# Kernel optimization log

Measured on AMD Instinct MI355X. Metric: run time of the kernel, lower is better.

Reference implementation:

```python
import jax, jax.numpy as jnp
import numpy as np

N = 100000   # nodes
E = 3200000  # edges (before self-loops)
G = 256      # graphs in batch
IN_DIM, HID, OUT3 = 25, 64, 32


def setup_inputs() -> dict:
    key = jax.random.key(0)
    ks = jax.random.split(key, 13)
    def w(k, shape, fan_in):
        return jax.random.normal(k, shape, jnp.float32) * (1.0 / np.sqrt(fan_in))
    return {
        "x": jax.random.normal(ks[0], (N, IN_DIM), jnp.float32),
        "edge_index": jax.random.randint(ks[1], (2, E), 0, N, dtype=jnp.int32),
        "batch": jnp.sort(jax.random.randint(ks[2], (N,), 0, G, dtype=jnp.int32)),
        "W1": w(ks[3], (IN_DIM, HID), IN_DIM), "b1": jnp.zeros((HID,), jnp.float32),
        "W2": w(ks[4], (HID, HID), HID),       "b2": jnp.zeros((HID,), jnp.float32),
        "W3": w(ks[5], (HID, OUT3), HID),      "b3": jnp.zeros((OUT3,), jnp.float32),
        "Wh1": w(ks[6], (OUT3, 32), OUT3),     "bh1": jnp.zeros((32,), jnp.float32),
        "Wh2": w(ks[7], (32, 1), 32),          "bh2": jnp.zeros((1,), jnp.float32),
    }


def _gcn_layer(x, W, b, src, dst, num_nodes):
    # GCNConv: h = W^T x; out_i = sum_j norm_ij * h_j (+ self-loop), norm = d_i^-1/2 d_j^-1/2
    h = x @ W  # [N, F_out]
    ones = jnp.ones(src.shape[0], h.dtype)
    deg = jax.ops.segment_sum(ones, dst, num_segments=num_nodes)  # includes self-loops -> >= 1
    dinv = jax.lax.rsqrt(jnp.maximum(deg, 1.0))
    norm = dinv[src] * dinv[dst]                       # [E+N]
    msgs = h[src] * norm[:, None]                       # gather + scale
    out = jax.ops.segment_sum(msgs, dst, num_segments=num_nodes)  # scatter-add
    return out + b


def reference(x, edge_index, batch, W1, b1, W2, b2, W3, b3, Wh1, bh1, Wh2, bh2):
    n = x.shape[0]
    loops = jnp.arange(n, dtype=edge_index.dtype)
    src = jnp.concatenate([edge_index[0], loops])  # add self-loops
    dst = jnp.concatenate([edge_index[1], loops])

    h = jax.nn.relu(_gcn_layer(x, W1, b1, src, dst, n))
    h = jax.nn.relu(_gcn_layer(h, W2, b2, src, dst, n))
    h = jax.nn.relu(_gcn_layer(h, W3, b3, src, dst, n))

    # global mean pool over graphs
    counts = jax.ops.segment_sum(jnp.ones(n, h.dtype), batch, num_segments=G)
    g = jax.ops.segment_sum(h, batch, num_segments=G) / jnp.maximum(counts, 1.0)[:, None]

    y = jax.nn.relu(g @ Wh1 + bh1) @ Wh2 + bh2  # [G, 1]
    return y.squeeze(-1)
```

## Files before the change

kernel.cpp:

```cpp
#include <hip/hip_runtime.h>
#include <hip/hip_fp16.h>


#define IN_DIM 25
#define HID 64
#define OUT3 32
#define BK_LOG 6
#define BK_NODES 64
#define MAXB 2048
#define NPT 8
#define EPB1 16384
#define BCAP 4096
#define RNG_LOG 14
#define NR 8
#define NKEY (BK_NODES * NR)

__global__ __launch_bounds__(256) void bucket_hist(const int* __restrict__ dst,
                                                   int* __restrict__ bhist, int nE) {
    __shared__ int h[MAXB];
    for (int i = threadIdx.x; i < MAXB; i += 256) h[i] = 0;
    __syncthreads();
    int e0 = blockIdx.x * 8192;
    int cnt = min(8192, nE - e0);
    for (int i = threadIdx.x; i < cnt; i += 256)
        atomicAdd(&h[(unsigned)dst[e0 + i] >> BK_LOG], 1);
    __syncthreads();
    for (int i = threadIdx.x; i < MAXB; i += 256)
        if (h[i]) atomicAdd(&bhist[i], h[i]);
}

__global__ __launch_bounds__(256) void bucket_scan(const int* __restrict__ bhist,
                                                   int* __restrict__ bbase,
                                                   int* __restrict__ cursor,
                                                   int nb, int nE) {
    __shared__ int s4[256];
    int t = threadIdx.x;
    int v[NPT]; int sum = 0;
#pragma unroll
    for (int j = 0; j < NPT; ++j) {
        int b = NPT * t + j;
        v[j] = (b < nb) ? bhist[b] : 0;
        sum += v[j];
    }
    s4[t] = sum;
    __syncthreads();
    for (int off = 1; off < 256; off <<= 1) {
        int mine = s4[t];
        int add = (t >= off) ? s4[t - off] : 0;
        __syncthreads();
        s4[t] = mine + add;
        __syncthreads();
    }
    int run = s4[t] - sum;
#pragma unroll
    for (int j = 0; j < NPT; ++j) {
        int b = NPT * t + j;
        if (b < nb) { bbase[b] = run; cursor[b] = run; }
        run += v[j];
    }
    if (t == 0) bbase[nb] = nE;
}

__global__ __launch_bounds__(256) void partition_kernel(
        const int* __restrict__ src, const int* __restrict__ dst,
        int* __restrict__ cursor, unsigned int* __restrict__ ebuf, int nE) {
    __shared__ int lh[MAXB];
    __shared__ int lrun[MAXB];
    __shared__ int lcur[MAXB];
    __shared__ int swp[256];
    __shared__ unsigned int stg[EPB1];
    __shared__ unsigned short sbk[EPB1];
    int t = threadIdx.x;
    int e0 = blockIdx.x * EPB1;
    int cnt = min(EPB1, nE - e0);
    for (int i = t; i < MAXB; i += 256) lh[i] = 0;
    __syncthreads();
    for (int i = t; i < cnt; i += 256)
        atomicAdd(&lh[(unsigned)dst[e0 + i] >> BK_LOG], 1);
    __syncthreads();
    int v[NPT]; int sum = 0;
#pragma unroll
    for (int j = 0; j < NPT; ++j) { v[j] = lh[NPT * t + j]; sum += v[j]; }
    swp[t] = sum;
    __syncthreads();
    for (int off = 1; off < 256; off <<= 1) {
        int mine = swp[t];
        int add = (t >= off) ? swp[t - off] : 0;
        __syncthreads();
        swp[t] = mine + add;
        __syncthreads();
    }
    int run = swp[t] - sum;
#pragma unroll
    for (int j = 0; j < NPT; ++j) {
        int b = NPT * t + j;
        lh[b] = run;
        lcur[b] = 0;
        if (v[j] > 0) lrun[b] = atomicAdd(&cursor[b], v[j]);
        run += v[j];
    }
    __syncthreads();
    for (int i = t; i < cnt; i += 256) {
        int d = dst[e0 + i];
        int s = src[e0 + i];
        int b = (unsigned)d >> BK_LOG;
        int lp = atomicAdd(&lcur[b], 1);
        int slot = lh[b] + lp;
        stg[slot] = ((unsigned)(d & (BK_NODES - 1)) << 17) | (unsigned)s;
        sbk[slot] = (unsigned short)b;
    }
    __syncthreads();
    for (int i = t; i < cnt; i += 256) {
        int b = sbk[i];
        int g = lrun[b] + (i - lh[b]);
        ebuf[g] = stg[i];
    }
}

__global__ __launch_bounds__(256) void bucket_csr_kernel(
        unsigned int* __restrict__ ebuf, const int* __restrict__ bbase,
        float* __restrict__ dinv, int* __restrict__ gp64, int* __restrict__ gp32,
        int nN) {
    int b = blockIdx.x;
    int node_lo = b << BK_LOG;
    int nn = min(BK_NODES, nN - node_lo);
    int base = bbase[b];
    int cnt = bbase[b + 1] - base;
    if (cnt > BCAP) cnt = BCAP;
    __shared__ unsigned int in[BCAP];
    __shared__ unsigned int outb[BCAP];
    __shared__ int h[NKEY], sc[NKEY], lc[NKEY];
    __shared__ int swp[256];
    int t = threadIdx.x;
    for (int i = t; i < cnt; i += 256) in[i] = ebuf[base + i];
    for (int i = t; i < NKEY; i += 256) { h[i] = 0; lc[i] = 0; }
    __syncthreads();
    for (int i = t; i < cnt; i += 256) {
        unsigned int w = in[i];
        int kk = (int)(((w & 0x1FFFFu) >> RNG_LOG) << BK_LOG) | (int)(w >> 17);
        atomicAdd(&h[kk], 1);
    }
    __syncthreads();
    int v[2]; int sum = 0;
#pragma unroll
    for (int j = 0; j < 2; ++j) { v[j] = h[2 * t + j]; sum += v[j]; }
    swp[t] = sum;
    __syncthreads();
    for (int off = 1; off < 256; off <<= 1) {
        int mine = swp[t];
        int add = (t >= off) ? swp[t - off] : 0;
        __syncthreads();
        swp[t] = mine + add;
        __syncthreads();
    }
    int run = swp[t] - sum;
#pragma unroll
    for (int j = 0; j < 2; ++j) { sc[2 * t + j] = run; run += v[j]; }
    __syncthreads();
    if (t < 64)  gp64[b * 65 + t]  = base + sc[((t >> 3) << BK_LOG) | ((t & 7)  << 3)];
    if (t < 128) gp32[b * 129 + t] = base + sc[((t >> 4) << BK_LOG) | ((t & 15) << 2)];
    if (t == 0) { gp64[b * 65 + 64] = base + cnt; gp32[b * 129 + 128] = base + cnt; }
    if (t < nn) {
        int deg = 0;
#pragma unroll
        for (int r = 0; r < NR; ++r) deg += h[(r << BK_LOG) | t];
        dinv[node_lo + t] = rsqrtf((float)deg + 1.0f);
    }
    __syncthreads();
    for (int i = t; i < cnt; i += 256) {
        unsigned int w = in[i];
        int kk = (int)(((w & 0x1FFFFu) >> RNG_LOG) << BK_LOG) | (int)(w >> 17);
        int lp = atomicAdd(&lc[kk], 1);
        outb[sc[kk] + lp] = w;
    }
    __syncthreads();
    for (int i = t; i < cnt; i += 256) ebuf[base + i] = outb[i];
}

__global__ void padx_kernel(const float* __restrict__ x, const float* __restrict__ dinv,
                            __half* __restrict__ xp, int n) {
    int i = blockIdx.x * 256 + threadIdx.x;
    if (i < n * 16) {
        int node = i >> 4, c2 = (i & 15) * 2;
        float s = dinv[node];
        float v0 = (c2     < IN_DIM) ? x[(size_t)node * IN_DIM + c2    ] * s : 0.f;
        float v1 = (c2 + 1 < IN_DIM) ? x[(size_t)node * IN_DIM + c2 + 1] * s : 0.f;
        *(__half2*)&xp[(size_t)node * 32 + c2] = __floats2half2_rn(v0, v1);
    }
}

__global__ void padw_kernel(const float* __restrict__ W1, float* __restrict__ W1p) {
    int i = blockIdx.x * 256 + threadIdx.x;
    if (i < 32 * HID) {
        int r = i >> 6, c = i & 63;
        W1p[i] = (r < IN_DIM) ? W1[r * HID + c] : 0.f;
    }
}

template<int INF, int OUTF, bool ACT, bool SCALE>
__global__ __launch_bounds__(256) void gemm_kernel(
        const float* __restrict__ in, const float* __restrict__ W,
        const float* __restrict__ bias, const float* __restrict__ dinv,
        void* __restrict__ out, int n) {
    constexpr int TPN = OUTF / 4;
    constexpr int NPB = 256 / TPN;
    constexpr int LDK = INF + 4;
    __shared__ float sW[INF * OUTF];
    __shared__ float sIn[NPB][LDK];
    for (int i = threadIdx.x; i < INF * OUTF; i += 256) sW[i] = W[i];
    int node0 = blockIdx.x * NPB;
    for (int i = threadIdx.x; i < NPB * INF; i += 256) {
        int ln = i / INF, k = i % INF;
        int node = node0 + ln;
        sIn[ln][k] = (node < n) ? in[(size_t)node * INF + k] : 0.f;
    }
    __syncthreads();
    int g   = threadIdx.x / TPN;
    int of0 = (threadIdx.x % TPN) * 4;
    int node = node0 + g;
    float4 acc = make_float4(0.f, 0.f, 0.f, 0.f);
#pragma unroll
    for (int k = 0; k < INF; ++k) {
        float aj = sIn[g][k];
        const float4 wv = *(const float4*)&sW[k * OUTF + of0];
        acc.x += aj * wv.x; acc.y += aj * wv.y;
        acc.z += aj * wv.z; acc.w += aj * wv.w;
    }
    if (ACT) {
        const float4 bv = *(const float4*)&bias[of0];
        acc.x = fmaxf(acc.x + bv.x, 0.f);
        acc.y = fmaxf(acc.y + bv.y, 0.f);
        acc.z = fmaxf(acc.z + bv.z, 0.f);
        acc.w = fmaxf(acc.w + bv.w, 0.f);
    }
    if (node < n) {
        if (SCALE) {
            float s = dinv[node];
            union { __half2 h[2]; uint2 u; } pk;
            pk.h[0] = __floats2half2_rn(acc.x * s, acc.y * s);
            pk.h[1] = __floats2half2_rn(acc.z * s, acc.w * s);
            *(uint2*)((__half*)out + (size_t)node * OUTF + of0) = pk.u;
        } else {
            *(float4*)((float*)out + (size_t)node * OUTF + of0) = acc;
        }
    }
}

template<int F, bool ACT>
__global__ __launch_bounds__(256, 6) void gatherp_kernel(
        const __half* __restrict__ hp, const float* __restrict__ dinv,
        const int* __restrict__ gp, const unsigned int* __restrict__ eb,
        const float* __restrict__ bias, float* __restrict__ agg, int n) {
    constexpr int LPN = F / 2;
    constexpr int G   = 256 / LPN;
    constexpr int GPB = NR * G + 1;
    __shared__ float acc[(BK_NODES + 1) * F];
    int b = blockIdx.x, t = threadIdx.x;
    int node_lo = b << BK_LOG;
    for (int i = t; i < BK_NODES * LPN; i += 256) {
        int ln = i / LPN, c2 = (i % LPN) * 2;
        int node = node_lo + ln;
        float2 v = make_float2(0.f, 0.f);
        if (node < n)
            v = __half22float2(*(const __half2*)&hp[(size_t)node * F + c2]);
        acc[ln * F + c2] = v.x;
        acc[ln * F + c2 + 1] = v.y;
    }
    __syncthreads();
    int g  = t / LPN;
    int c2 = (t % LPN) * 2;
    float ax = 0.f, ay = 0.f;
    int cur = BK_NODES;
    for (int r = 0; r < NR; ++r) {
        int e  = gp[b * GPB + r * G + g];
        int e1 = gp[b * GPB + r * G + g + 1];
        for (; e + 8 <= e1; e += 8) {
            unsigned int w[8];
#pragma unroll
            for (int u = 0; u < 8; ++u) w[u] = eb[e + u];
            float2 v[8];
#pragma unroll
            for (int u = 0; u < 8; ++u)
                v[u] = __half22float2(
                    *(const __half2*)&hp[(size_t)(w[u] & 0x1FFFFu) * F + c2]);
#pragma unroll
            for (int u = 0; u < 8; ++u) {
                int dl = (int)(w[u] >> 17);
                if (dl != cur) {
                    acc[cur * F + c2]     += ax;
                    acc[cur * F + c2 + 1] += ay;
                    ax = 0.f; ay = 0.f; cur = dl;
                }
                ax += v[u].x; ay += v[u].y;
            }
        }
        for (; e < e1; ++e) {
            unsigned int w = eb[e];
            float2 v = __half22float2(
                *(const __half2*)&hp[(size_t)(w & 0x1FFFFu) * F + c2]);
            int dl = (int)(w >> 17);
            if (dl != cur) {
                acc[cur * F + c2]     += ax;
                acc[cur * F + c2 + 1] += ay;
                ax = 0.f; ay = 0.f; cur = dl;
            }
            ax += v.x; ay += v.y;
        }
        acc[cur * F + c2]     += ax;
        acc[cur * F + c2 + 1] += ay;
        ax = 0.f; ay = 0.f; cur = BK_NODES;
        __syncthreads();
    }
    for (int i = t; i < BK_NODES * LPN; i += 256) {
        int ln = i / LPN, cc = (i % LPN) * 2;
        int node = node_lo + ln;
        if (node < n) {
            float s = dinv[node];
            float rx = acc[ln * F + cc] * s;
            float ry = acc[ln * F + cc + 1] * s;
            if (ACT) {
                rx = fmaxf(rx + bias[cc], 0.f);
                ry = fmaxf(ry + bias[cc + 1], 0.f);
            }
            union { float2 f; unsigned long long u; } o;
            o.f = make_float2(rx, ry);
            __builtin_nontemporal_store(o.u,
                (unsigned long long*)&agg[(size_t)node * F + cc]);
        }
    }
}

__global__ __launch_bounds__(256) void pool_kernel(
        const float* __restrict__ h3, const int* __restrict__ batch,
        int n, float* __restrict__ pool) {
    int g = blockIdx.x;
    int lo = 0, hi = n;
    while (lo < hi) { int m = (lo + hi) >> 1; if (batch[m] < g) lo = m + 1; else hi = m; }
    int s = lo;
    hi = n;
    while (lo < hi) { int m = (lo + hi) >> 1; if (batch[m] < g + 1) lo = m + 1; else hi = m; }
    int e = lo;
    constexpr int F = OUT3;
    int ln = threadIdx.x / F;
    int f  = threadIdx.x % F;
    float acc = 0.f;
    for (int i = s + ln; i < e; i += 8)
        acc += h3[(size_t)i * F + f];
    __shared__ float red[8][F];
    red[ln][f] = acc;
    __syncthreads();
    if (ln == 0) {
        float t = 0.f;
#pragma unroll
        for (int j = 0; j < 8; ++j) t += red[j][f];
        float cnt = (float)((e - s) > 0 ? (e - s) : 1);
        pool[g * F + f] = t / cnt;
    }
}

__global__ __launch_bounds__(256) void head_kernel(
        const float* __restrict__ pool, const float* __restrict__ Wh1,
        const float* __restrict__ bh1, const float* __restrict__ Wh2,
        const float* __restrict__ bh2, float* __restrict__ out) {
    __shared__ float sW1[32 * 32];
    __shared__ float sb1[32];
    __shared__ float sW2[32];
    int t = threadIdx.x;
    for (int i = t; i < 1024; i += 256) sW1[i] = Wh1[i];
    if (t < 32) { sb1[t] = bh1[t]; sW2[t] = Wh2[t]; }
    __syncthreads();
    int g = t;
    float y = bh2[0];
    const float* p = &pool[g * 32];
#pragma unroll 4
    for (int j = 0; j < 32; ++j) {
        float a = sb1[j];
#pragma unroll
        for (int k = 0; k < 32; ++k) a += p[k] * sW1[k * 32 + j];
        y += fmaxf(a, 0.f) * sW2[j];
    }
    out[g] = y;
}

extern "C" void kernel_launch(void* const* d_in, const int* in_sizes, int n_in,
                              void* d_out, int out_size, void* d_ws, size_t ws_size,
                              hipStream_t stream) {
    const float* x    = (const float*)d_in[0];
    const int*   ei   = (const int*)  d_in[1];
    const int*   batch= (const int*)  d_in[2];
    const float* W1   = (const float*)d_in[3];
    const float* b1   = (const float*)d_in[4];
    const float* W2   = (const float*)d_in[5];
    const float* b2   = (const float*)d_in[6];
    const float* W3   = (const float*)d_in[7];
    const float* b3   = (const float*)d_in[8];
    const float* Wh1  = (const float*)d_in[9];
    const float* bh1  = (const float*)d_in[10];
    const float* Wh2  = (const float*)d_in[11];
    const float* bh2  = (const float*)d_in[12];
    float* out = (float*)d_out;

    const int N = in_sizes[0] / IN_DIM;
    const int E = in_sizes[1] / 2;
    const int* src = ei;
    const int* dst = ei + E;
    const int NB = (N + BK_NODES - 1) >> BK_LOG;

    char* base = (char*)d_ws;
    unsigned int* ebuf = (unsigned int*)base;       base += (size_t)E * 4;
    int*   bhist   = (int*)base;                    base += (size_t)MAXB * 4;
    int*   bbase   = (int*)base;                    base += (size_t)(MAXB + 1) * 4;
    int*   cursor  = (int*)base;                    base += (size_t)MAXB * 4;
    int*   gp64    = (int*)base;                    base += (size_t)MAXB * 65 * 4;
    int*   gp32    = (int*)base;                    base += (size_t)MAXB * 129 * 4;
    float* dinv    = (float*)base;                  base += (size_t)N * 4;
    float* W1p     = (float*)base;                  base += (size_t)32 * HID * 4;
    float* bufA    = (float*)base;                  base += (size_t)N * HID * 4;
    float* bufB    = (float*)base;                  base += (size_t)N * HID * 4;
    float* pool    = (float*)base;

    hipMemsetAsync(bhist, 0, (size_t)MAXB * sizeof(int), stream);
    bucket_hist<<<(E + 8191) / 8192, 256, 0, stream>>>(dst, bhist, E);
    bucket_scan<<<1, 256, 0, stream>>>(bhist, bbase, cursor, NB, E);
    partition_kernel<<<(E + EPB1 - 1) / EPB1, 256, 0, stream>>>(src, dst, cursor, ebuf, E);
    bucket_csr_kernel<<<NB, 256, 0, stream>>>(ebuf, bbase, dinv, gp64, gp32, N);

    padx_kernel<<<((size_t)N * 16 + 255) / 256, 256, 0, stream>>>(x, dinv, (__half*)bufB, N);
    padw_kernel<<<(32 * HID + 255) / 256, 256, 0, stream>>>(W1, W1p);
    gatherp_kernel<32, false><<<NB, 256, 0, stream>>>((const __half*)bufB, dinv, gp32, ebuf, nullptr, bufA, N);
    gemm_kernel<32, HID, true, false><<<(N + 15) / 16, 256, 0, stream>>>(bufA, W1p, b1, nullptr, bufB, N);

    gemm_kernel<HID, HID, false, true><<<(N + 15) / 16, 256, 0, stream>>>(bufB, W2, nullptr, dinv, bufA, N);
    gatherp_kernel<64, true><<<NB, 256, 0, stream>>>((const __half*)bufA, dinv, gp64, ebuf, b2, bufB, N);

    gemm_kernel<HID, OUT3, false, true><<<(N + 31) / 32, 256, 0, stream>>>(bufB, W3, nullptr, dinv, bufA, N);
    gatherp_kernel<32, true><<<NB, 256, 0, stream>>>((const __half*)bufA, dinv, gp32, ebuf, b3, bufB, N);

    pool_kernel<<<256, 256, 0, stream>>>(bufB, batch, N, pool);
    head_kernel<<<1, 256, 0, stream>>>(pool, Wh1, bh1, Wh2, bh2, out);
}
```

Before: 474.0 us.

## Simplify edge partition: register-held edges, direct scatter, smaller blocks

The partition kernel now holds each thread's 16 edges in registers instead of reloading dst/src from global memory. It also drops the local prefix scan and the shared-memory staging buffer, writing each edge straight to its global bucket slot with a nontemporal store. Smaller blocks (4096 edges) use less LDS, which allows more concurrent blocks. The trade-off is uncoalesced scattered global writes and four times as many global cursor atomics.

After: 524.7 us. +10.7%, slower.

```diff
diff --git a/kernel.cpp b/kernel.cpp
--- a/kernel.cpp
+++ b/kernel.cpp
@@ -9,7 +9,8 @@
 #define BK_NODES 64
 #define MAXB 2048
 #define NPT 8
-#define EPB1 16384
+#define EPB1 4096
+#define EPT 16
 #define BCAP 4096
 #define RNG_LOG 14
 #define NR 8
@@ -66,54 +67,36 @@
         int* __restrict__ cursor, unsigned int* __restrict__ ebuf, int nE) {
     __shared__ int lh[MAXB];
     __shared__ int lrun[MAXB];
-    __shared__ int lcur[MAXB];
-    __shared__ int swp[256];
-    __shared__ unsigned int stg[EPB1];
-    __shared__ unsigned short sbk[EPB1];
     int t = threadIdx.x;
     int e0 = blockIdx.x * EPB1;
     int cnt = min(EPB1, nE - e0);
     for (int i = t; i < MAXB; i += 256) lh[i] = 0;
     __syncthreads();
-    for (int i = t; i < cnt; i += 256)
-        atomicAdd(&lh[(unsigned)dst[e0 + i] >> BK_LOG], 1);
-    __syncthreads();
-    int v[NPT]; int sum = 0;
-#pragma unroll
-    for (int j = 0; j < NPT; ++j) { v[j] = lh[NPT * t + j]; sum += v[j]; }
-    swp[t] = sum;
-    __syncthreads();
-    for (int off = 1; off < 256; off <<= 1) {
-        int mine = swp[t];
-        int add = (t >= off) ? swp[t - off] : 0;
-        __syncthreads();
-        swp[t] = mine + add;
-        __syncthreads();
-    }
-    int run = swp[t] - sum;
-#pragma unroll
-    for (int j = 0; j < NPT; ++j) {
-        int b = NPT * t + j;
-        lh[b] = run;
-        lcur[b] = 0;
-        if (v[j] > 0) lrun[b] = atomicAdd(&cursor[b], v[j]);
-        run += v[j];
-    }
-    __syncthreads();
-    for (int i = t; i < cnt; i += 256) {
-        int d = dst[e0 + i];
-        int s = src[e0 + i];
-        int b = (unsigned)d >> BK_LOG;
-        int lp = atomicAdd(&lcur[b], 1);
-        int slot = lh[b] + lp;
-        stg[slot] = ((unsigned)(d & (BK_NODES - 1)) << 17) | (unsigned)s;
-        sbk[slot] = (unsigned short)b;
-    }
-    __syncthreads();
-    for (int i = t; i < cnt; i += 256) {
-        int b = sbk[i];
-        int g = lrun[b] + (i - lh[b]);
-        ebuf[g] = stg[i];
+    int d[EPT], s[EPT];
+#pragma unroll
+    for (int j = 0; j < EPT; ++j) {
+        int i = t + j * 256;
+        if (i < cnt) {
+            d[j] = dst[e0 + i];
+            s[j] = src[e0 + i];
+            atomicAdd(&lh[(unsigned)d[j] >> BK_LOG], 1);
+        } else d[j] = -1;
+    }
+    __syncthreads();
+    for (int b = t; b < MAXB; b += 256) {
+        int v = lh[b];
+        lh[b] = 0;
+        if (v > 0) lrun[b] = atomicAdd(&cursor[b], v);
+    }
+    __syncthreads();
+#pragma unroll
+    for (int j = 0; j < EPT; ++j) {
+        if (d[j] >= 0) {
+            int b = (unsigned)d[j] >> BK_LOG;
+            int lp = atomicAdd(&lh[b], 1);
+            unsigned int w = ((unsigned)(d[j] & (BK_NODES - 1)) << 17) | (unsigned)s[j];
+            __builtin_nontemporal_store(w, &ebuf[lrun[b] + lp]);
+        }
     }
 }
 
```
